# Kernel optimization log

Measured on AMD Instinct MI355X. Metric: run time of the kernel, lower is better.

The kernel has to match this reference:

```python
import jax, jax.numpy as jnp
import numpy as np

B, N, T, H, P = 512, 128, 336, 32, 1  # batch, nodes, seq_len, hidden, pred_len


def setup_inputs() -> dict:
    key = jax.random.key(0)
    ks = jax.random.split(key, 9)
    s = 1.0 / np.sqrt(H)  # torch LSTM/Linear init bound
    u = lambda k, shape: jax.random.uniform(k, shape, dtype=jnp.float32, minval=-s, maxval=s)
    return {
        "x": jax.random.normal(ks[0], (B, N, T), dtype=jnp.float32),
        # layer 0: input_size=1
        "W_ih0": u(ks[1], (N, 4 * H, 1)),
        "W_hh0": u(ks[2], (N, 4 * H, H)),
        "b0": u(ks[3], (N, 4 * H)),  # = b_ih0 + b_hh0 (additive in the cell)
        # layer 1: input_size=H
        "W_ih1": u(ks[4], (N, 4 * H, H)),
        "W_hh1": u(ks[5], (N, 4 * H, H)),
        "b1": u(ks[6], (N, 4 * H)),
        # per-node linear head
        "W_fc": u(ks[7], (N, P, H)),
        "b_fc": u(ks[8], (N, P)),
    }


def _cell(x_proj, h, c, W_hh, b):
    # x_proj, h, c: [B, N, H*(...)]; torch gate order: i, f, g, o
    gates = x_proj + jnp.einsum("bnh,ngh->bng", h, W_hh) + b
    i, f, g, o = jnp.split(gates, 4, axis=-1)
    c = jax.nn.sigmoid(f) * c + jax.nn.sigmoid(i) * jnp.tanh(g)
    h = jax.nn.sigmoid(o) * jnp.tanh(c)
    return h, c


def reference(x, W_ih0, W_hh0, b0, W_ih1, W_hh1, b1, W_fc, b_fc):
    Bx, Nx, Tx = x.shape
    Hx = W_hh0.shape[-1]
    Wi0 = W_ih0[:, :, 0]  # [N, 4H] since input_size == 1
    xs = jnp.moveaxis(x, 2, 0)  # [T, B, N]
    zeros = jnp.zeros((Bx, Nx, Hx), x.dtype)
    init = (zeros, zeros, zeros, zeros)  # h0, c0, h1, c1

    def step(carry, x_t):
        h0, c0, h1, c1 = carry
        xp0 = x_t[:, :, None] * Wi0[None]          # [B, N, 4H]
        h0, c0 = _cell(xp0, h0, c0, W_hh0, b0)
        xp1 = jnp.einsum("bnh,ngh->bng", h0, W_ih1)
        h1, c1 = _cell(xp1, h1, c1, W_hh1, b1)
        return (h0, c0, h1, c1), None

    (h0, c0, h1, c1), _ = jax.lax.scan(step, init, xs)
    # last-timestep top-layer hidden through per-node linear head
    return jnp.einsum("bnh,nph->bnp", h1, W_fc) + b_fc[None]
```

## Files before the change

kernel.cpp:

```cpp
#include <hip/hip_runtime.h>
#include <stdint.h>

#define NB 512
#define NN 128
#define NT 336
#define NH 32
#define NG 128

typedef short bf16x8 __attribute__((ext_vector_type(8)));
typedef float f32x4  __attribute__((ext_vector_type(4)));
typedef float f32x2  __attribute__((ext_vector_type(2)));
typedef float f32v4  __attribute__((ext_vector_type(4)));

#define LOG2E 1.4426950408889634f
#define KNEG  (-2.0f * LOG2E)

__device__ __forceinline__ f32x2 exp2v(f32x2 v) {
  f32x2 r; r.x = __builtin_amdgcn_exp2f(v.x); r.y = __builtin_amdgcn_exp2f(v.y); return r;
}
__device__ __forceinline__ f32x2 rcpv(f32x2 v) {
  f32x2 r; r.x = __builtin_amdgcn_rcpf(v.x); r.y = __builtin_amdgcn_rcpf(v.y); return r;
}
__device__ __forceinline__ short f2bf(float f) {
  unsigned u = __builtin_bit_cast(unsigned, f) + 0x8000u;
  return (short)(u >> 16);
}

template<bool BIAS>
__device__ __forceinline__ f32x2 cell_pair(f32x2 gi, f32x2 gf, f32x2 gg, f32x2 go,
                                           f32x2& cst, float ebi, float ebf,
                                           float ebg, float kng, float ebo) {
  f32x2 wi = exp2v(gi), wf = exp2v(gf), uu = exp2v(gg), wo = exp2v(go);
  f32x2 Ai, Af, Au, Ao, nuk;
  if (BIAS) {
    Ai  = wi * ebi + 1.0f;
    Af  = wf * ebf + 1.0f;
    Au  = uu * ebg + 1.0f;
    Ao  = wo * ebo + 1.0f;
    nuk = uu * kng + KNEG;
  } else {
    Ai  = wi + 1.0f; Af = wf + 1.0f; Au = uu + 1.0f; Ao = wo + 1.0f;
    nuk = uu * (-KNEG) + KNEG;
  }
  f32x2 P  = Ai * Au;
  f32x2 N  = cst * P + nuk * Af;
  f32x2 cS = N * rcpv(Af * P);
  cst = cS;
  f32x2 sarg = cS;
  sarg.x = fminf(sarg.x, 80.0f);
  sarg.y = fminf(sarg.y, 80.0f);
  f32x2 vv = exp2v(sarg);
  f32x2 hh = (1.0f - vv) * rcpv(Ao * (vv + 1.0f));
  return hh;
}

__global__ __launch_bounds__(256, 2) void lstm_kernel(
    const float* __restrict__ x,
    const float* __restrict__ Wih0,
    const float* __restrict__ Whh0,
    const float* __restrict__ b0,
    const float* __restrict__ Wih1,
    const float* __restrict__ Whh1,
    const float* __restrict__ b1,
    const float* __restrict__ Wfc,
    const float* __restrict__ bfc,
    float* __restrict__ out)
{
  const int tid  = threadIdx.x;
  const int wave = tid >> 6;
  const int lane = tid & 63;
  const int c    = lane & 15;
  const int q    = lane >> 4;
  const int n    = blockIdx.x >> 3;
  const int m0   = ((blockIdx.x & 7) * 4 + wave) * 16;

  __shared__ short lds[4 * 2 * 16 * 40];
  short* my0 = lds + wave * (2 * 16 * 40);
  short* my1 = my0 + 16 * 40;

  const float sc_tab[8] = {-LOG2E, -LOG2E, -LOG2E, -LOG2E,
                           -2.0f * LOG2E, -2.0f * LOG2E, -LOG2E, -LOG2E};

  bf16x8 wb0[8], wb1[8], wb2[8];
  {
    const float* pW0 = Whh0 + n * (NG * NH);
    const float* pW1 = Wih1 + n * (NG * NH);
    const float* pW2 = Whh1 + n * (NG * NH);
#pragma unroll
    for (int tau = 0; tau < 8; ++tau) {
      int off = (tau * 16 + c) * NH + q * 8;
      float sc = sc_tab[tau];
#pragma unroll
      for (int j = 0; j < 8; ++j) {
        wb0[tau][j] = f2bf(sc * pW0[off + j]);
        wb1[tau][j] = f2bf(sc * pW1[off + j]);
        wb2[tau][j] = f2bf(sc * pW2[off + j]);
      }
    }
  }
  float b0g[8], eb1[8], wi0g[8];
#pragma unroll
  for (int tau = 0; tau < 8; ++tau) {
    int g = tau * 16 + c;
    float sc = sc_tab[tau];
    b0g[tau]  = sc * b0[n * NG + g];
    eb1[tau]  = __builtin_amdgcn_exp2f(sc * b1[n * NG + g]);
    wi0g[tau] = sc * Wih0[n * NG + g];
  }
  const float kng4 = (-KNEG) * eb1[4];
  const float kng5 = (-KNEG) * eb1[5];
  const float wfc0 = Wfc[n * NH + c];
  const float wfc1 = Wfc[n * NH + 16 + c];

  const float* px0 = x + ((size_t)(m0 + q * 4 + 0) * NN + n) * NT;
  const float* px1 = x + ((size_t)(m0 + q * 4 + 1) * NN + n) * NT;
  const float* px2 = x + ((size_t)(m0 + q * 4 + 2) * NN + n) * NT;
  const float* px3 = x + ((size_t)(m0 + q * 4 + 3) * NN + n) * NT;

  bf16x8 a0 = {0,0,0,0,0,0,0,0};
  bf16x8 a1 = {0,0,0,0,0,0,0,0};
  f32x2 c0p[2][2], c1p[2][2];
#pragma unroll
  for (int tu = 0; tu < 2; ++tu)
#pragma unroll
    for (int p = 0; p < 2; ++p) {
      c0p[tu][p] = (f32x2){0.f, 0.f};
      c1p[tu][p] = (f32x2){0.f, 0.f};
    }

  const f32x4 zero4 = {0.f, 0.f, 0.f, 0.f};

  f32v4 xb0 = *(const f32v4*)(px0);
  f32v4 xb1 = *(const f32v4*)(px1);
  f32v4 xb2 = *(const f32v4*)(px2);
  f32v4 xb3 = *(const f32v4*)(px3);

#pragma unroll 1
  for (int t4 = 0; t4 < NT / 4; ++t4) {
    const int tn = (t4 + 1 < NT / 4) ? (t4 + 1) * 4 : t4 * 4;
    f32v4 xn0 = *(const f32v4*)(px0 + tn);
    f32v4 xn1 = *(const f32v4*)(px1 + tn);
    f32v4 xn2 = *(const f32v4*)(px2 + tn);
    f32v4 xn3 = *(const f32v4*)(px3 + tn);

#pragma unroll
    for (int ts = 0; ts < 4; ++ts) {
      f32x2 x01 = {xb0[ts], xb1[ts]};
      f32x2 x23 = {xb2[ts], xb3[ts]};

      f32x4 acc[8];
#pragma unroll
      for (int tau = 0; tau < 8; ++tau) {
        f32x2 w2 = {wi0g[tau], wi0g[tau]};
        f32x2 b2 = {b0g[tau], b0g[tau]};
        f32x2 lo = x01 * w2 + b2;
        f32x2 hi = x23 * w2 + b2;
        acc[tau] = (f32x4){lo.x, lo.y, hi.x, hi.y};
      }
#pragma unroll
      for (int tau = 0; tau < 8; ++tau)
        acc[tau] = __builtin_amdgcn_mfma_f32_16x16x32_bf16(a0, wb0[tau], acc[tau], 0, 0, 0);

#pragma unroll
      for (int tu = 0; tu < 2; ++tu) {
#pragma unroll
        for (int p = 0; p < 2; ++p) {
          f32x2 gi = { acc[tu    ][2*p], acc[tu    ][2*p+1] };
          f32x2 gf = { acc[tu + 2][2*p], acc[tu + 2][2*p+1] };
          f32x2 gg = { acc[tu + 4][2*p], acc[tu + 4][2*p+1] };
          f32x2 go = { acc[tu + 6][2*p], acc[tu + 6][2*p+1] };
          f32x2 hh = cell_pair<false>(gi, gf, gg, go, c0p[tu][p],
                                      1.f, 1.f, 1.f, 1.f, 1.f);
          my0[(q * 4 + 2*p    ) * 40 + tu * 16 + c] = f2bf(hh.x);
          my0[(q * 4 + 2*p + 1) * 40 + tu * 16 + c] = f2bf(hh.y);
        }
      }
      asm volatile("" ::: "memory");

#pragma unroll
      for (int tau = 0; tau < 8; ++tau)
        acc[tau] = __builtin_amdgcn_mfma_f32_16x16x32_bf16(a1, wb2[tau], zero4, 0, 0, 0);

      a0 = *(const bf16x8*)(my0 + c * 40 + q * 8);

#pragma unroll
      for (int tau = 0; tau < 8; ++tau)
        acc[tau] = __builtin_amdgcn_mfma_f32_16x16x32_bf16(a0, wb1[tau], acc[tau], 0, 0, 0);

#pragma unroll
      for (int tu = 0; tu < 2; ++tu) {
#pragma unroll
        for (int p = 0; p < 2; ++p) {
          f32x2 gi = { acc[tu    ][2*p], acc[tu    ][2*p+1] };
          f32x2 gf = { acc[tu + 2][2*p], acc[tu + 2][2*p+1] };
          f32x2 gg = { acc[tu + 4][2*p], acc[tu + 4][2*p+1] };
          f32x2 go = { acc[tu + 6][2*p], acc[tu + 6][2*p+1] };
          f32x2 hh = cell_pair<true>(gi, gf, gg, go, c1p[tu][p],
                                     eb1[tu], eb1[tu + 2], eb1[tu + 4],
                                     (tu == 0) ? kng4 : kng5, eb1[tu + 6]);
          my1[(q * 4 + 2*p    ) * 40 + tu * 16 + c] = f2bf(hh.x);
          my1[(q * 4 + 2*p + 1) * 40 + tu * 16 + c] = f2bf(hh.y);
        }
      }
      asm volatile("" ::: "memory");
      a1 = *(const bf16x8*)(my1 + c * 40 + q * 8);
    }

    xb0 = xn0; xb1 = xn1; xb2 = xn2; xb3 = xn3;
  }

  float h1v[2][4];
#pragma unroll
  for (int tu = 0; tu < 2; ++tu)
#pragma unroll
    for (int r = 0; r < 4; ++r) {
      unsigned short us = (unsigned short)my1[(q * 4 + r) * 40 + tu * 16 + c];
      h1v[tu][r] = __builtin_bit_cast(float, ((unsigned)us) << 16);
    }
  float s0 = h1v[0][0] * wfc0 + h1v[1][0] * wfc1;
  float s1 = h1v[0][1] * wfc0 + h1v[1][1] * wfc1;
  float s2 = h1v[0][2] * wfc0 + h1v[1][2] * wfc1;
  float s3 = h1v[0][3] * wfc0 + h1v[1][3] * wfc1;
#pragma unroll
  for (int off = 1; off < 16; off <<= 1) {
    s0 += __shfl_xor(s0, off, 64);
    s1 += __shfl_xor(s1, off, 64);
    s2 += __shfl_xor(s2, off, 64);
    s3 += __shfl_xor(s3, off, 64);
  }
  if (c < 4) {
    float v = (c == 0) ? s0 : (c == 1) ? s1 : (c == 2) ? s2 : s3;
    out[(size_t)(m0 + q * 4 + c) * NN + n] = v + bfc[n];
  }
}

extern "C" void kernel_launch(void* const* d_in, const int* in_sizes, int n_in,
                              void* d_out, int out_size, void* d_ws, size_t ws_size,
                              hipStream_t stream) {
  const float* x    = (const float*)d_in[0];
  const float* Wih0 = (const float*)d_in[1];
  const float* Whh0 = (const float*)d_in[2];
  const float* b0   = (const float*)d_in[3];
  const float* Wih1 = (const float*)d_in[4];
  const float* Whh1 = (const float*)d_in[5];
  const float* b1   = (const float*)d_in[6];
  const float* Wfc  = (const float*)d_in[7];
  const float* bfc  = (const float*)d_in[8];
  float* out = (float*)d_out;

  lstm_kernel<<<dim3(1024), dim3(256), 0, stream>>>(
      x, Wih0, Whh0, b0, Wih1, Whh1, b1, Wfc, bfc, out);
}
```

Before: 1.336 ms.

## Pin LSTM weights in AGPRs, drop x prefetch, reorder layer-1 MFMAs

Forces the three bf16 weight fragment arrays into accumulation registers (AGPRs) through inline asm constraints, which frees VGPRs for the recurrent state. The one-step-ahead prefetch of x is removed and each 4-step chunk is now loaded at the top of its iteration. In layer 1 the h0·W_ih1 MFMAs now run first and the h1·W_hh1 MFMAs accumulate onto them, with empty asm barriers on the accumulators to fix the schedule. The aim is lower register pressure and better MFMA scheduling, at the cost of exposing global-load latency for x at each chunk and possible AGPR-to-VGPR operand moves.

Measured after the change: 2.589 ms. 1.94x slower.

```diff
diff --git a/kernel.cpp b/kernel.cpp
--- a/kernel.cpp
+++ b/kernel.cpp
@@ -98,6 +98,13 @@
       }
     }
   }
+#pragma unroll
+  for (int tau = 0; tau < 8; ++tau) {
+    asm volatile("" : "+a"(wb0[tau]));
+    asm volatile("" : "+a"(wb1[tau]));
+    asm volatile("" : "+a"(wb2[tau]));
+  }
+
   float b0g[8], eb1[8], wi0g[8];
 #pragma unroll
   for (int tau = 0; tau < 8; ++tau) {
@@ -130,23 +137,17 @@
 
   const f32x4 zero4 = {0.f, 0.f, 0.f, 0.f};
 
-  f32v4 xb0 = *(const f32v4*)(px0);
-  f32v4 xb1 = *(const f32v4*)(px1);
-  f32v4 xb2 = *(const f32v4*)(px2);
-  f32v4 xb3 = *(const f32v4*)(px3);
-
 #pragma unroll 1
   for (int t4 = 0; t4 < NT / 4; ++t4) {
-    const int tn = (t4 + 1 < NT / 4) ? (t4 + 1) * 4 : t4 * 4;
-    f32v4 xn0 = *(const f32v4*)(px0 + tn);
-    f32v4 xn1 = *(const f32v4*)(px1 + tn);
-    f32v4 xn2 = *(const f32v4*)(px2 + tn);
-    f32v4 xn3 = *(const f32v4*)(px3 + tn);
+    f32v4 xr0 = *(const f32v4*)(px0 + t4 * 4);
+    f32v4 xr1 = *(const f32v4*)(px1 + t4 * 4);
+    f32v4 xr2 = *(const f32v4*)(px2 + t4 * 4);
+    f32v4 xr3 = *(const f32v4*)(px3 + t4 * 4);
 
 #pragma unroll
     for (int ts = 0; ts < 4; ++ts) {
-      f32x2 x01 = {xb0[ts], xb1[ts]};
-      f32x2 x23 = {xb2[ts], xb3[ts]};
+      f32x2 x01 = {xr0[ts], xr1[ts]};
+      f32x2 x23 = {xr2[ts], xr3[ts]};
 
       f32x4 acc[8];
 #pragma unroll
@@ -158,8 +159,10 @@
         acc[tau] = (f32x4){lo.x, lo.y, hi.x, hi.y};
       }
 #pragma unroll
-      for (int tau = 0; tau < 8; ++tau)
+      for (int tau = 0; tau < 8; ++tau) {
         acc[tau] = __builtin_amdgcn_mfma_f32_16x16x32_bf16(a0, wb0[tau], acc[tau], 0, 0, 0);
+        asm volatile("" : "+v"(acc[tau]));
+      }
 
 #pragma unroll
       for (int tu = 0; tu < 2; ++tu) {
@@ -176,16 +179,16 @@
         }
       }
       asm volatile("" ::: "memory");
+      a0 = *(const bf16x8*)(my0 + c * 40 + q * 8);
 
 #pragma unroll
       for (int tau = 0; tau < 8; ++tau)
-        acc[tau] = __builtin_amdgcn_mfma_f32_16x16x32_bf16(a1, wb2[tau], zero4, 0, 0, 0);
-
-      a0 = *(const bf16x8*)(my0 + c * 40 + q * 8);
-
-#pragma unroll
-      for (int tau = 0; tau < 8; ++tau)
-        acc[tau] = __builtin_amdgcn_mfma_f32_16x16x32_bf16(a0, wb1[tau], acc[tau], 0, 0, 0);
+        acc[tau] = __builtin_amdgcn_mfma_f32_16x16x32_bf16(a0, wb1[tau], zero4, 0, 0, 0);
+#pragma unroll
+      for (int tau = 0; tau < 8; ++tau) {
+        acc[tau] = __builtin_amdgcn_mfma_f32_16x16x32_bf16(a1, wb2[tau], acc[tau], 0, 0, 0);
+        asm volatile("" : "+v"(acc[tau]));
+      }
 
 #pragma unroll
       for (int tu = 0; tu < 2; ++tu) {
@@ -205,8 +208,6 @@
       asm volatile("" ::: "memory");
       a1 = *(const bf16x8*)(my1 + c * 40 + q * 8);
     }
-
-    xb0 = xn0; xb1 = xn1; xb2 = xn2; xb3 = xn3;
   }
 
   float h1v[2][4];
```
